# Kernel optimization log

Measured on AMD Instinct MI355X. Metric: run time of the kernel, lower is better.

## Reference

```python
import jax, jax.numpy as jnp
import numpy as np


def _pool2(x):
    # 2x2 max pool, stride 2 (matches F.max_pool2d(x, 2))
    b, c, h, w = x.shape
    return x.reshape(b, c, h // 2, 2, w // 2, 2).max(axis=(3, 5))


def setup_inputs() -> dict:
    key = jax.random.key(0)
    ks = jax.random.split(key, 6)
    B, C, H, W = 16, 512, 64, 64
    x = jax.random.normal(ks[0], (B, C, H, W), dtype=jnp.float32)
    scale = 0.02
    theta_w = jax.random.normal(ks[1], (C // 8, C), dtype=jnp.float32) * scale
    phi_w = jax.random.normal(ks[2], (C // 8, C), dtype=jnp.float32) * scale
    g_w = jax.random.normal(ks[3], (C // 2, C), dtype=jnp.float32) * scale
    o_w = jax.random.normal(ks[4], (C, C // 2), dtype=jnp.float32) * scale
    # original inits gamma=0; use a nonzero value so output depends on attention path
    gamma = jax.random.normal(ks[5], (), dtype=jnp.float32) * 0.5
    return {"x": x, "theta_w": theta_w, "phi_w": phi_w, "g_w": g_w, "o_w": o_w, "gamma": gamma}


def reference(x, theta_w, phi_w, g_w, o_w, gamma):
    B, C, H, W = x.shape
    HW = H * W
    # 1x1 convs == channel GEMMs
    theta = jnp.einsum('bchw,kc->bkhw', x, theta_w).reshape(B, C // 8, HW).transpose(0, 2, 1)  # [B, HW, C/8]
    phi = _pool2(jnp.einsum('bchw,kc->bkhw', x, phi_w)).reshape(B, C // 8, HW // 4)            # [B, C/8, HW/4]
    beta = jax.nn.softmax(jnp.einsum('bnk,bkm->bnm', theta, phi), axis=-1)                     # [B, HW, HW/4]
    g = _pool2(jnp.einsum('bchw,kc->bkhw', x, g_w)).reshape(B, C // 2, HW // 4)                # [B, C/2, HW/4]
    # g.bmm(beta^T): contract over pooled positions m -> [B, C/2, HW]
    o_in = jnp.einsum('bcm,bnm->bcn', g, beta).reshape(B, C // 2, H, W)
    o = jnp.einsum('bchw,kc->bkhw', o_in, o_w)                                                 # [B, C, H, W]
    return gamma * o + x
```

## Files before the change

### kernel.cpp

```cpp
#include <hip/hip_runtime.h>

#define B_   16
#define C_   512
#define HW_  4096
#define M_   1024
#define TPAD 136

typedef __attribute__((ext_vector_type(8))) short bf16x8;
typedef __attribute__((ext_vector_type(4))) float f32x4;

static __device__ __forceinline__ unsigned short f2bf(float f) {
    union { float f; unsigned u; } v; v.f = f;
    unsigned r = v.u + 0x7fffu + ((v.u >> 16) & 1u);
    return (unsigned short)(r >> 16);
}
static __device__ __forceinline__ float bf2f(unsigned short h) {
    union { unsigned u; float f; } v; v.u = ((unsigned)h) << 16;
    return v.f;
}
static __device__ __forceinline__ void gload_lds16(const void* g, void* l) {
    __builtin_amdgcn_global_load_lds(
        (const __attribute__((address_space(1))) unsigned int*)g,
        (__attribute__((address_space(3))) unsigned int*)l, 16, 0, 0);
}
static __device__ __forceinline__ int fb(int row) { return (row ^ (row >> 2)) & 7; }

__global__ __launch_bounds__(256) void k_weights(
    const float* __restrict__ thw, const float* __restrict__ phw,
    const float* __restrict__ gw,  const float* __restrict__ ow,
    unsigned short* __restrict__ Wb, unsigned short* __restrict__ oWb,
    unsigned short* __restrict__ g_p) {
    int i = blockIdx.x * 256 + threadIdx.x;
    if (i < 32768)        Wb[i] = f2bf(thw[i]);
    else if (i < 65536)   Wb[i] = f2bf(phw[i - 32768]);
    else if (i < 196608)  Wb[i] = f2bf(gw[i - 65536]);
    else if (i < 327680)  oWb[i - 196608] = f2bf(ow[i - 196608]);
    else if (i < 589824) {
        int i2 = i - 327680;
        int b = i2 >> 14;
        int r = (i2 >> 10) & 15;
        int m = i2 & 1023;
        g_p[((size_t)b * 272 + 256 + r) * M_ + m] =
            (r == 0) ? (unsigned short)0x3F80u : (unsigned short)0;
    }
}

__global__ __launch_bounds__(256, 2) void k_proj(
    const float* __restrict__ x, const unsigned short* __restrict__ Wb,
    unsigned short* __restrict__ theta_n, unsigned short* __restrict__ phi_p,
    unsigned short* __restrict__ g_p) {
    __shared__ unsigned short smem[128 * TPAD];
    unsigned short* Bs0 = smem;
    unsigned short* Bs1 = smem + 8192;

    int b = blockIdx.z, mt = blockIdx.y, bx = blockIdx.x;
    int hw0 = bx * 128;
    int tid = threadIdx.x, w = tid >> 6, lane = tid & 63;
    int l15 = lane & 15, q = lane >> 4;
    int wr = w >> 1, wc = w & 1;

    const unsigned short* Ab = Wb + (size_t)(mt * 128) * 512;
    const float* xb = x + (size_t)b * C_ * HW_ + hw0;
    int hg4 = (tid & 31) * 4;
    int kq2 = (tid >> 5) * 2;

    float4 breg[8];

#define LOADB(k0v)                                                             \
    _Pragma("unroll")                                                          \
    for (int it = 0; it < 2; it++) {                                           \
        int kg = kq2 + it;                                                     \
        const float* xs = xb + (size_t)((k0v) + kg * 4) * HW_ + hg4;           \
        breg[it * 4 + 0] = *reinterpret_cast<const float4*>(xs);               \
        breg[it * 4 + 1] = *reinterpret_cast<const float4*>(xs + HW_);         \
        breg[it * 4 + 2] = *reinterpret_cast<const float4*>(xs + 2 * HW_);     \
        breg[it * 4 + 3] = *reinterpret_cast<const float4*>(xs + 3 * HW_);     \
    }

#define WRITEB(dst)                                                            \
    _Pragma("unroll")                                                          \
    for (int it = 0; it < 2; it++) {                                           \
        int kg = kq2 + it;                                                     \
        _Pragma("unroll")                                                      \
        for (int t = 0; t < 4; t++) {                                          \
            int row = hg4 + t;                                                 \
            int ch = (kg >> 1) ^ fb(row);                                      \
            ushort4 u;                                                         \
            u.x = f2bf(((const float*)&breg[it * 4 + 0])[t]);                  \
            u.y = f2bf(((const float*)&breg[it * 4 + 1])[t]);                  \
            u.z = f2bf(((const float*)&breg[it * 4 + 2])[t]);                  \
            u.w = f2bf(((const float*)&breg[it * 4 + 3])[t]);                  \
            *reinterpret_cast<ushort4*>(&(dst)[row * 64 + ch * 8 + (kg & 1) * 4]) = u; \
        }                                                                      \
    }

    LOADB(0);
    WRITEB(Bs0);

    f32x4 acc[4][4] = {};
#pragma unroll
    for (int ks = 0; ks < 8; ks++) {
        int k0 = ks * 64;
        unsigned short* cur = (ks & 1) ? Bs1 : Bs0;
        unsigned short* nxt = (ks & 1) ? Bs0 : Bs1;
        __syncthreads();
        bf16x8 af[2][4];
#pragma unroll
        for (int kk = 0; kk < 2; kk++)
#pragma unroll
            for (int mi = 0; mi < 4; mi++) {
                int row = wr * 64 + mi * 16 + l15;
                af[kk][mi] = *(const bf16x8*)(Ab + (size_t)row * 512 + k0 + kk * 32 + q * 8);
            }
        if (ks < 7) { LOADB(k0 + 64); }
#pragma unroll
        for (int kk = 0; kk < 2; kk++) {
            bf16x8 bfr[4];
#pragma unroll
            for (int ni = 0; ni < 4; ni++) {
                int row = wc * 64 + ni * 16 + l15;
                int ch = (kk * 4 + q) ^ fb(row);
                bfr[ni] = *(const bf16x8*)&cur[row * 64 + ch * 8];
            }
#pragma unroll
            for (int mi = 0; mi < 4; mi++)
#pragma unroll
                for (int ni = 0; ni < 4; ni++)
                    acc[mi][ni] = __builtin_amdgcn_mfma_f32_16x16x32_bf16(
                        af[kk][mi], bfr[ni], acc[mi][ni], 0, 0, 0);
        }
        if (ks < 7) { WRITEB(nxt); }
    }
#undef LOADB
#undef WRITEB

    __syncthreads();
#pragma unroll
    for (int mi = 0; mi < 4; mi++)
#pragma unroll
        for (int ni = 0; ni < 4; ni++) {
            int col = wc * 64 + ni * 16 + l15;
            int row = wr * 64 + mi * 16 + q * 4;
            ushort4 u;
            u.x = f2bf(acc[mi][ni][0]); u.y = f2bf(acc[mi][ni][1]);
            u.z = f2bf(acc[mi][ni][2]); u.w = f2bf(acc[mi][ni][3]);
            *reinterpret_cast<ushort4*>(&smem[col * TPAD + row]) = u;
        }
    __syncthreads();

    if (mt == 0) {
        int hw_l = tid >> 1, kh = (tid & 1) * 32;
        const unsigned short* srcp = &smem[hw_l * TPAD + kh];
        unsigned short* dstp = theta_n + ((size_t)b * HW_ + hw0 + hw_l) * 64 + kh;
#pragma unroll
        for (int i = 0; i < 4; i++)
            *reinterpret_cast<uint4*>(dstp + i * 8) =
                *reinterpret_cast<const uint4*>(srcp + i * 8);
        int pc = tid & 63, mg = tid >> 6;
#pragma unroll
        for (int j = 0; j < 8; j++) {
            int m_l = mg * 8 + j, w_ = m_l * 2;
            float v0 = bf2f(smem[(w_)      * TPAD + 64 + pc]);
            float v1 = bf2f(smem[(w_ + 1)  * TPAD + 64 + pc]);
            float v2 = bf2f(smem[(64 + w_) * TPAD + 64 + pc]);
            float v3 = bf2f(smem[(65 + w_) * TPAD + 64 + pc]);
            float v = fmaxf(fmaxf(v0, v1), fmaxf(v2, v3));
            phi_p[((size_t)b * M_ + bx * 32 + m_l) * 64 + pc] = f2bf(v);
        }
    } else {
        int lr = tid & 127, half = tid >> 7;
        int gc = (mt - 1) * 128 + lr;
        unsigned short* dst = g_p + ((size_t)b * 272 + gc) * M_ + bx * 32 + half * 16;
        unsigned short tmp[16];
#pragma unroll
        for (int i = 0; i < 16; i++) {
            int w_ = (half * 16 + i) * 2;
            float v0 = bf2f(smem[(w_)      * TPAD + lr]);
            float v1 = bf2f(smem[(w_ + 1)  * TPAD + lr]);
            float v2 = bf2f(smem[(64 + w_) * TPAD + lr]);
            float v3 = bf2f(smem[(65 + w_) * TPAD + lr]);
            tmp[i] = f2bf(fmaxf(fmaxf(v0, v1), fmaxf(v2, v3)));
        }
#pragma unroll
        for (int i = 0; i < 4; i++)
            *reinterpret_cast<ushort4*>(dst + i * 4) =
                *reinterpret_cast<const ushort4*>(&tmp[i * 4]);
    }
}

__global__ __launch_bounds__(512, 4) void k_attn(
    const unsigned short* __restrict__ theta_n, const unsigned short* __restrict__ phi_p,
    const unsigned short* __restrict__ g_p, unsigned short* __restrict__ o_in) {
    __shared__ unsigned short phi_s[64 * 64];
    __shared__ unsigned short g_s[272 * 64];
    __shared__ unsigned short p_lds[8][16][88];

    int b = blockIdx.y, n0 = blockIdx.x * 128;
    int tid = threadIdx.x, w = tid >> 6, lane = tid & 63;
    int l15 = lane & 15, q = lane >> 4;
    int nw = n0 + w * 16;

    const unsigned short* th = theta_n + ((size_t)b * HW_ + nw + l15) * 64 + q * 8;
    bf16x8 a0 = *(const bf16x8*)(th);
    bf16x8 a1 = *(const bf16x8*)(th + 32);

    const unsigned short* phib = phi_p + (size_t)b * M_ * 64;
    const unsigned short* gb   = g_p   + (size_t)b * 272 * M_;

    int sw = l15 & 7;

    f32x4 acc[17] = {};
    for (int mc = 0; mc < 16; mc++) {
        int m0 = mc * 64;
        __syncthreads();
        {
            int p = tid;
            int row = p >> 3, ch = (p & 7) ^ (row & 7);
            gload_lds16(phib + (size_t)(m0 + row) * 64 + ch * 8, &phi_s[w * 512]);
        }
#pragma unroll
        for (int it = 0; it < 5; it++) {
            int s = w + it * 8;
            if (s < 34) {
                int row = s * 8 + (lane >> 3);
                int ch = (lane & 7) ^ (row & 7);
                gload_lds16(gb + (size_t)row * M_ + m0 + ch * 8, &g_s[s * 512]);
            }
        }
        __syncthreads();

#pragma unroll
        for (int f = 0; f < 4; f++) {
            const unsigned short* pr = &phi_s[(f * 16 + l15) * 64];
            bf16x8 b0 = *(const bf16x8*)(pr + (q ^ sw) * 8);
            bf16x8 b1 = *(const bf16x8*)(pr + ((q + 4) ^ sw) * 8);
            f32x4 s = {};
            s = __builtin_amdgcn_mfma_f32_16x16x32_bf16(a0, b0, s, 0, 0, 0);
            s = __builtin_amdgcn_mfma_f32_16x16x32_bf16(a1, b1, s, 0, 0, 0);
#pragma unroll
            for (int j = 0; j < 4; j++)
                p_lds[w][q * 4 + j][f * 16 + l15] = f2bf(__expf(s[j]));
        }
        bf16x8 p0 = *(const bf16x8*)&p_lds[w][l15][q * 8];
        bf16x8 p1 = *(const bf16x8*)&p_lds[w][l15][32 + q * 8];
#pragma unroll
        for (int cf = 0; cf < 17; cf++) {
            const unsigned short* gr = &g_s[(cf * 16 + l15) * 64];
            bf16x8 g0 = *(const bf16x8*)(gr + (q ^ sw) * 8);
            bf16x8 g1 = *(const bf16x8*)(gr + ((q + 4) ^ sw) * 8);
            acc[cf] = __builtin_amdgcn_mfma_f32_16x16x32_bf16(p0, g0, acc[cf], 0, 0, 0);
            acc[cf] = __builtin_amdgcn_mfma_f32_16x16x32_bf16(p1, g1, acc[cf], 0, 0, 0);
        }
    }

    float dinv[4];
#pragma unroll
    for (int j = 0; j < 4; j++) {
        float d = __shfl(acc[16][j], (lane & 48), 64);
        dinv[j] = 1.0f / d;
    }
#pragma unroll
    for (int cf = 0; cf < 16; cf++)
#pragma unroll
        for (int j = 0; j < 4; j++)
            o_in[((size_t)b * HW_ + nw + q * 4 + j) * 256 + cf * 16 + l15] =
                f2bf(acc[cf][j] * dinv[j]);
}

__global__ __launch_bounds__(256, 4) void k_oproj(
    const unsigned short* __restrict__ o_in, const unsigned short* __restrict__ oWb,
    const float* __restrict__ x, const float* __restrict__ gamma_p,
    float* __restrict__ out) {
    __shared__ unsigned short smem[128 * TPAD];
    unsigned short* As = smem;
    unsigned short* Bs = smem + 8192;

    int b = blockIdx.z, mt = blockIdx.y, hw0 = blockIdx.x * 128;
    int tid = threadIdx.x, w = tid >> 6, lane = tid & 63;
    int l15 = lane & 15, q = lane >> 4;
    int wr = w >> 1, wc = w & 1;

    const unsigned short* Ab = oWb + (size_t)(mt * 128) * 256;
    const unsigned short* Bb = o_in + ((size_t)b * HW_ + hw0) * 256;
    int trow = tid >> 3, tch = tid & 7;

    f32x4 acc[4][4] = {};
    for (int ks = 0; ks < 4; ks++) {
        int k0 = ks * 64;
        if (ks) __syncthreads();
#pragma unroll
        for (int i = 0; i < 4; i++) {
            int row = i * 32 + trow;
            int ch = tch ^ (row & 7);
            gload_lds16(Ab + (size_t)row * 256 + k0 + ch * 8, &As[(i * 256 + w * 64) * 8]);
        }
#pragma unroll
        for (int i = 0; i < 4; i++) {
            int row = i * 32 + trow;
            int ch = tch ^ (row & 7);
            gload_lds16(Bb + (size_t)row * 256 + k0 + ch * 8, &Bs[(i * 256 + w * 64) * 8]);
        }
        __syncthreads();
#pragma unroll
        for (int kk = 0; kk < 2; kk++) {
            bf16x8 af[4], bfr[4];
#pragma unroll
            for (int mi = 0; mi < 4; mi++) {
                int row = wr * 64 + mi * 16 + l15;
                int ch = (kk * 4 + q) ^ (row & 7);
                af[mi] = *(const bf16x8*)&As[row * 64 + ch * 8];
            }
#pragma unroll
            for (int ni = 0; ni < 4; ni++) {
                int row = wc * 64 + ni * 16 + l15;
                int ch = (kk * 4 + q) ^ (row & 7);
                bfr[ni] = *(const bf16x8*)&Bs[row * 64 + ch * 8];
            }
#pragma unroll
            for (int mi = 0; mi < 4; mi++)
#pragma unroll
                for (int ni = 0; ni < 4; ni++)
                    acc[mi][ni] = __builtin_amdgcn_mfma_f32_16x16x32_bf16(
                        af[mi], bfr[ni], acc[mi][ni], 0, 0, 0);
        }
    }

    __syncthreads();
#pragma unroll
    for (int mi = 0; mi < 4; mi++)
#pragma unroll
        for (int ni = 0; ni < 4; ni++) {
            int col = wc * 64 + ni * 16 + l15;
            int rb = wr * 64 + mi * 16 + q * 4;
#pragma unroll
            for (int j = 0; j < 4; j++)
                smem[(rb + j) * TPAD + col] = f2bf(acc[mi][ni][j]);
        }
    __syncthreads();

    float gam = *gamma_p;
    int sub = tid >> 5, p32 = tid & 31;
#pragma unroll
    for (int p = 0; p < 16; p++) {
        int row = p * 8 + sub;
        ushort4 v = *reinterpret_cast<const ushort4*>(&smem[row * TPAD + p32 * 4]);
        size_t idx = ((size_t)b * C_ + mt * 128 + row) * HW_ + hw0 + p32 * 4;
        float4 xv = *reinterpret_cast<const float4*>(x + idx);
        float4 o;
        o.x = gam * bf2f(v.x) + xv.x;
        o.y = gam * bf2f(v.y) + xv.y;
        o.z = gam * bf2f(v.z) + xv.z;
        o.w = gam * bf2f(v.w) + xv.w;
        *reinterpret_cast<float4*>(out + idx) = o;
    }
}

extern "C" void kernel_launch(void* const* d_in, const int* in_sizes, int n_in,
                              void* d_out, int out_size, void* d_ws, size_t ws_size,
                              hipStream_t stream) {
    const float* x     = (const float*)d_in[0];
    const float* thw   = (const float*)d_in[1];
    const float* phw   = (const float*)d_in[2];
    const float* gw    = (const float*)d_in[3];
    const float* ow    = (const float*)d_in[4];
    const float* gamma = (const float*)d_in[5];
    float* out = (float*)d_out;

    char* ws = (char*)d_ws;
    unsigned short* Wb   = (unsigned short*)(ws + 0);
    unsigned short* oWb  = (unsigned short*)(ws + 393216);
    unsigned short* oin  = (unsigned short*)(ws + 655360);
    unsigned short* thn  = (unsigned short*)(ws + 34209792);
    unsigned short* phip = (unsigned short*)(ws + 42598400);
    unsigned short* gp   = (unsigned short*)(ws + 44695552);

    hipLaunchKernelGGL(k_weights, dim3(2304), dim3(256), 0, stream, thw, phw, gw, ow, Wb, oWb, gp);
    hipLaunchKernelGGL(k_proj, dim3(32, 3, 16), dim3(256), 0, stream, x, Wb, thn, phip, gp);
    hipLaunchKernelGGL(k_attn, dim3(32, 16), dim3(512), 0, stream, thn, phip, gp, oin);
    hipLaunchKernelGGL(k_oproj, dim3(32, 4, 16), dim3(256), 0, stream, oin, oWb, x, gamma, out);
}
```

Measured before the change: 189.1 us.

## Compute all 384 projection channels per block to read x once

The projection kernel now covers all three weight tiles (theta/phi plus both g halves, 384 rows) in one 512-thread block instead of three separate blocks along grid y. Each x tile is loaded and converted to bf16 once rather than three times, which cuts global reads of the large fp32 input. The epilogue then loops over the three 128-row tiles, staging each through LDS. The cost is fewer blocks (512 versus 1536), more accumulator registers per thread (24 fragments), and extra barriers in the epilogue.

Result: slower. 195.7 us (+3.5%).

```diff
diff --git a/kernel.cpp b/kernel.cpp
--- a/kernel.cpp
+++ b/kernel.cpp
@@ -45,7 +45,7 @@
     }
 }
 
-__global__ __launch_bounds__(256, 2) void k_proj(
+__global__ __launch_bounds__(512, 2) void k_proj(
     const float* __restrict__ x, const unsigned short* __restrict__ Wb,
     unsigned short* __restrict__ theta_n, unsigned short* __restrict__ phi_p,
     unsigned short* __restrict__ g_p) {
@@ -53,138 +53,130 @@
     unsigned short* Bs0 = smem;
     unsigned short* Bs1 = smem + 8192;
 
-    int b = blockIdx.z, mt = blockIdx.y, bx = blockIdx.x;
+    int b = blockIdx.y, bx = blockIdx.x;
     int hw0 = bx * 128;
     int tid = threadIdx.x, w = tid >> 6, lane = tid & 63;
     int l15 = lane & 15, q = lane >> 4;
-    int wr = w >> 1, wc = w & 1;
-
-    const unsigned short* Ab = Wb + (size_t)(mt * 128) * 512;
+    int rg = w >> 1, cg = w & 1;
+
     const float* xb = x + (size_t)b * C_ * HW_ + hw0;
     int hg4 = (tid & 31) * 4;
-    int kq2 = (tid >> 5) * 2;
-
-    float4 breg[8];
+    int kg  = tid >> 5;
+
+    float4 breg[4];
 
 #define LOADB(k0v)                                                             \
-    _Pragma("unroll")                                                          \
-    for (int it = 0; it < 2; it++) {                                           \
-        int kg = kq2 + it;                                                     \
+    {                                                                          \
         const float* xs = xb + (size_t)((k0v) + kg * 4) * HW_ + hg4;           \
-        breg[it * 4 + 0] = *reinterpret_cast<const float4*>(xs);               \
-        breg[it * 4 + 1] = *reinterpret_cast<const float4*>(xs + HW_);         \
-        breg[it * 4 + 2] = *reinterpret_cast<const float4*>(xs + 2 * HW_);     \
-        breg[it * 4 + 3] = *reinterpret_cast<const float4*>(xs + 3 * HW_);     \
+        breg[0] = *reinterpret_cast<const float4*>(xs);                        \
+        breg[1] = *reinterpret_cast<const float4*>(xs + HW_);                  \
+        breg[2] = *reinterpret_cast<const float4*>(xs + 2 * HW_);              \
+        breg[3] = *reinterpret_cast<const float4*>(xs + 3 * HW_);              \
     }
 
 #define WRITEB(dst)                                                            \
     _Pragma("unroll")                                                          \
-    for (int it = 0; it < 2; it++) {                                           \
-        int kg = kq2 + it;                                                     \
-        _Pragma("unroll")                                                      \
-        for (int t = 0; t < 4; t++) {                                          \
-            int row = hg4 + t;                                                 \
-            int ch = (kg >> 1) ^ fb(row);                                      \
-            ushort4 u;                                                         \
-            u.x = f2bf(((const float*)&breg[it * 4 + 0])[t]);                  \
-            u.y = f2bf(((const float*)&breg[it * 4 + 1])[t]);                  \
-            u.z = f2bf(((const float*)&breg[it * 4 + 2])[t]);                  \
-            u.w = f2bf(((const float*)&breg[it * 4 + 3])[t]);                  \
-            *reinterpret_cast<ushort4*>(&(dst)[row * 64 + ch * 8 + (kg & 1) * 4]) = u; \
-        }                                                                      \
+    for (int t = 0; t < 4; t++) {                                              \
+        int row = hg4 + t;                                                     \
+        int ch = (kg >> 1) ^ fb(row);                                          \
+        ushort4 u;                                                             \
+        u.x = f2bf(((const float*)&breg[0])[t]);                               \
+        u.y = f2bf(((const float*)&breg[1])[t]);                               \
+        u.z = f2bf(((const float*)&breg[2])[t]);                               \
+        u.w = f2bf(((const float*)&breg[3])[t]);                               \
+        *reinterpret_cast<ushort4*>(&(dst)[row * 64 + ch * 8 + (kg & 1) * 4]) = u; \
     }
 
     LOADB(0);
     WRITEB(Bs0);
 
-    f32x4 acc[4][4] = {};
+    f32x4 acc[6][4] = {};
 #pragma unroll
     for (int ks = 0; ks < 8; ks++) {
         int k0 = ks * 64;
         unsigned short* cur = (ks & 1) ? Bs1 : Bs0;
         unsigned short* nxt = (ks & 1) ? Bs0 : Bs1;
         __syncthreads();
-        bf16x8 af[2][4];
-#pragma unroll
-        for (int kk = 0; kk < 2; kk++)
-#pragma unroll
-            for (int mi = 0; mi < 4; mi++) {
-                int row = wr * 64 + mi * 16 + l15;
-                af[kk][mi] = *(const bf16x8*)(Ab + (size_t)row * 512 + k0 + kk * 32 + q * 8);
-            }
         if (ks < 7) { LOADB(k0 + 64); }
 #pragma unroll
         for (int kk = 0; kk < 2; kk++) {
-            bf16x8 bfr[4];
+            bf16x8 af[6], bfr[4];
+#pragma unroll
+            for (int mi = 0; mi < 6; mi++) {
+                int row = rg * 96 + mi * 16 + l15;
+                af[mi] = *(const bf16x8*)(Wb + (size_t)row * 512 + k0 + kk * 32 + q * 8);
+            }
 #pragma unroll
             for (int ni = 0; ni < 4; ni++) {
-                int row = wc * 64 + ni * 16 + l15;
+                int row = cg * 64 + ni * 16 + l15;
                 int ch = (kk * 4 + q) ^ fb(row);
                 bfr[ni] = *(const bf16x8*)&cur[row * 64 + ch * 8];
             }
 #pragma unroll
-            for (int mi = 0; mi < 4; mi++)
+            for (int mi = 0; mi < 6; mi++)
 #pragma unroll
                 for (int ni = 0; ni < 4; ni++)
                     acc[mi][ni] = __builtin_amdgcn_mfma_f32_16x16x32_bf16(
-                        af[kk][mi], bfr[ni], acc[mi][ni], 0, 0, 0);
+                        af[mi], bfr[ni], acc[mi][ni], 0, 0, 0);
         }
         if (ks < 7) { WRITEB(nxt); }
     }
 #undef LOADB
 #undef WRITEB
 
-    __syncthreads();
-#pragma unroll
-    for (int mi = 0; mi < 4; mi++)
-#pragma unroll
-        for (int ni = 0; ni < 4; ni++) {
-            int col = wc * 64 + ni * 16 + l15;
-            int row = wr * 64 + mi * 16 + q * 4;
-            ushort4 u;
-            u.x = f2bf(acc[mi][ni][0]); u.y = f2bf(acc[mi][ni][1]);
-            u.z = f2bf(acc[mi][ni][2]); u.w = f2bf(acc[mi][ni][3]);
-            *reinterpret_cast<ushort4*>(&smem[col * TPAD + row]) = u;
-        }
-    __syncthreads();
-
-    if (mt == 0) {
-        int hw_l = tid >> 1, kh = (tid & 1) * 32;
-        const unsigned short* srcp = &smem[hw_l * TPAD + kh];
-        unsigned short* dstp = theta_n + ((size_t)b * HW_ + hw0 + hw_l) * 64 + kh;
-#pragma unroll
-        for (int i = 0; i < 4; i++)
-            *reinterpret_cast<uint4*>(dstp + i * 8) =
-                *reinterpret_cast<const uint4*>(srcp + i * 8);
-        int pc = tid & 63, mg = tid >> 6;
-#pragma unroll
-        for (int j = 0; j < 8; j++) {
-            int m_l = mg * 8 + j, w_ = m_l * 2;
-            float v0 = bf2f(smem[(w_)      * TPAD + 64 + pc]);
-            float v1 = bf2f(smem[(w_ + 1)  * TPAD + 64 + pc]);
-            float v2 = bf2f(smem[(64 + w_) * TPAD + 64 + pc]);
-            float v3 = bf2f(smem[(65 + w_) * TPAD + 64 + pc]);
-            float v = fmaxf(fmaxf(v0, v1), fmaxf(v2, v3));
-            phi_p[((size_t)b * M_ + bx * 32 + m_l) * 64 + pc] = f2bf(v);
-        }
-    } else {
-        int lr = tid & 127, half = tid >> 7;
-        int gc = (mt - 1) * 128 + lr;
-        unsigned short* dst = g_p + ((size_t)b * 272 + gc) * M_ + bx * 32 + half * 16;
-        unsigned short tmp[16];
-#pragma unroll
-        for (int i = 0; i < 16; i++) {
-            int w_ = (half * 16 + i) * 2;
-            float v0 = bf2f(smem[(w_)      * TPAD + lr]);
-            float v1 = bf2f(smem[(w_ + 1)  * TPAD + lr]);
-            float v2 = bf2f(smem[(64 + w_) * TPAD + lr]);
-            float v3 = bf2f(smem[(65 + w_) * TPAD + lr]);
-            tmp[i] = f2bf(fmaxf(fmaxf(v0, v1), fmaxf(v2, v3)));
-        }
-#pragma unroll
-        for (int i = 0; i < 4; i++)
-            *reinterpret_cast<ushort4*>(dst + i * 4) =
-                *reinterpret_cast<const ushort4*>(&tmp[i * 4]);
+    for (int t = 0; t < 3; t++) {
+        __syncthreads();
+#pragma unroll
+        for (int mi = 0; mi < 6; mi++) {
+            int grow = rg * 96 + mi * 16;
+            if ((grow >> 7) == t) {
+#pragma unroll
+                for (int ni = 0; ni < 4; ni++) {
+                    int col = cg * 64 + ni * 16 + l15;
+                    int row = (grow & 127) + q * 4;
+                    ushort4 u;
+                    u.x = f2bf(acc[mi][ni][0]); u.y = f2bf(acc[mi][ni][1]);
+                    u.z = f2bf(acc[mi][ni][2]); u.w = f2bf(acc[mi][ni][3]);
+                    *reinterpret_cast<ushort4*>(&smem[col * TPAD + row]) = u;
+                }
+            }
+        }
+        __syncthreads();
+
+        if (t == 0) {
+            int hw_l = tid >> 2, kh = (tid & 3) * 16;
+            const unsigned short* srcp = &smem[hw_l * TPAD + kh];
+            unsigned short* dstp = theta_n + ((size_t)b * HW_ + hw0 + hw_l) * 64 + kh;
+            *reinterpret_cast<uint4*>(dstp)     = *reinterpret_cast<const uint4*>(srcp);
+            *reinterpret_cast<uint4*>(dstp + 8) = *reinterpret_cast<const uint4*>(srcp + 8);
+            int pc = tid & 63, mg = tid >> 6;
+#pragma unroll
+            for (int j = 0; j < 4; j++) {
+                int m_l = mg * 4 + j, w_ = m_l * 2;
+                float v0 = bf2f(smem[(w_)      * TPAD + 64 + pc]);
+                float v1 = bf2f(smem[(w_ + 1)  * TPAD + 64 + pc]);
+                float v2 = bf2f(smem[(64 + w_) * TPAD + 64 + pc]);
+                float v3 = bf2f(smem[(65 + w_) * TPAD + 64 + pc]);
+                float v = fmaxf(fmaxf(v0, v1), fmaxf(v2, v3));
+                phi_p[((size_t)b * M_ + bx * 32 + m_l) * 64 + pc] = f2bf(v);
+            }
+        } else {
+            int lr = tid & 127, mq = tid >> 7;
+            int gc = (t - 1) * 128 + lr;
+            unsigned short* dst = g_p + ((size_t)b * 272 + gc) * M_ + bx * 32 + mq * 8;
+            unsigned short tmp[8];
+#pragma unroll
+            for (int i = 0; i < 8; i++) {
+                int w_ = (mq * 8 + i) * 2;
+                float v0 = bf2f(smem[(w_)      * TPAD + lr]);
+                float v1 = bf2f(smem[(w_ + 1)  * TPAD + lr]);
+                float v2 = bf2f(smem[(64 + w_) * TPAD + lr]);
+                float v3 = bf2f(smem[(65 + w_) * TPAD + lr]);
+                tmp[i] = f2bf(fmaxf(fmaxf(v0, v1), fmaxf(v2, v3)));
+            }
+            *reinterpret_cast<ushort4*>(dst)     = *reinterpret_cast<const ushort4*>(&tmp[0]);
+            *reinterpret_cast<ushort4*>(dst + 4) = *reinterpret_cast<const ushort4*>(&tmp[4]);
+        }
     }
 }
 
@@ -375,7 +367,7 @@
     unsigned short* gp   = (unsigned short*)(ws + 44695552);
 
     hipLaunchKernelGGL(k_weights, dim3(2304), dim3(256), 0, stream, thw, phw, gw, ow, Wb, oWb, gp);
-    hipLaunchKernelGGL(k_proj, dim3(32, 3, 16), dim3(256), 0, stream, x, Wb, thn, phip, gp);
+    hipLaunchKernelGGL(k_proj, dim3(32, 16), dim3(512), 0, stream, x, Wb, thn, phip, gp);
     hipLaunchKernelGGL(k_attn, dim3(32, 16), dim3(512), 0, stream, thn, phip, gp, oin);
     hipLaunchKernelGGL(k_oproj, dim3(32, 4, 16), dim3(256), 0, stream, oin, oWb, x, gamma, out);
 }
```
